# Optimization experiments

Hardware: AMD Instinct MI355X
Metric: run time of the kernel (lower is better)

The kernel has to match this reference:

```python
import jax, jax.numpy as jnp
import numpy as np

B, S, D = 4096, 200, 64
EPS = 1e-3  # keras BatchNormalization default epsilon

def setup_inputs() -> dict:
    key = jax.random.key(0)
    ks = jax.random.split(key, 8)
    return {
        "em": jax.random.normal(ks[0], (B, D), jnp.float32),
        "eu": jax.random.normal(ks[1], (B, D), jnp.float32),
        "Xu": jax.random.normal(ks[2], (B, S, D), jnp.float32),
        "W1": jax.random.normal(ks[3], (4 * D, 64), jnp.float32) * 0.05,
        "b1": jnp.zeros((64,), jnp.float32),
        "W2": jax.random.normal(ks[4], (64, 32), jnp.float32) * 0.1,
        "b2": jnp.zeros((32,), jnp.float32),
        "W3": jax.random.normal(ks[5], (32, 1), jnp.float32) * 0.1,
        "b3": jnp.zeros((1,), jnp.float32),
        "gamma": jnp.ones((2 * D,), jnp.float32),
        "beta": jnp.zeros((2 * D,), jnp.float32),
        "mov_mean": jnp.zeros((2 * D,), jnp.float32),
        "mov_var": jnp.ones((2 * D,), jnp.float32),
    }

def reference(em, eu, Xu, W1, b1, W2, b2, W3, b3, gamma, beta, mov_mean, mov_var):
    # DIN attention: query = em tiled over seq, key = value = Xu
    q = jnp.broadcast_to(em[:, None, :], Xu.shape)            # [B,S,D]
    info = jnp.concatenate([q, Xu, q - Xu, q * Xu], axis=-1)  # [B,S,4D]
    h = jax.nn.relu(info @ W1 + b1)                           # [B,S,64]
    h = jax.nn.relu(h @ W2 + b2)                              # [B,S,32]
    logits = (h @ W3 + b3)[..., 0]                            # [B,S]
    w = jax.nn.softmax(logits, axis=-1)                       # [B,S]
    pooled = jnp.einsum('bs,bsd->bd', w, Xu)                  # [B,D]
    info_all = jnp.concatenate([pooled, em], axis=-1)         # [B,2D]
    bn = (info_all - mov_mean) * jax.lax.rsqrt(mov_var + EPS) * gamma + beta
    return jnp.concatenate([bn, eu], axis=-1)                 # [B,2D+Du]
```

## Files before the change

### kernel.cpp

```cpp
#include <hip/hip_runtime.h>
#include <hip/hip_bf16.h>
#include <math.h>

typedef __bf16 bf16_t;
typedef bf16_t bf16x4 __attribute__((ext_vector_type(4)));
typedef bf16_t bf16x8 __attribute__((ext_vector_type(8)));
typedef float  f32x4  __attribute__((ext_vector_type(4)));

#define SEQ 200
#define SP  208
#define DD  64
#define RS  72

#define MFMA(a, b, c) __builtin_amdgcn_mfma_f32_16x16x32_bf16((a), (b), (c), 0, 0, 0)

__global__ __launch_bounds__(256) void prep_kernel(
    const float* __restrict__ em, const float* __restrict__ W1,
    const float* __restrict__ b1, const float* __restrict__ W2,
    bf16_t* __restrict__ Wbc, bf16_t* __restrict__ W1dt,
    bf16_t* __restrict__ W2t, float* __restrict__ Q)
{
  const int tid = threadIdx.x;
  if (blockIdx.x == 0) {
    for (int i = tid; i < 64 * 64; i += 256) {
      int n = i >> 6, k = i & 63;
      Wbc[i]  = (bf16_t)(W1[(64 + k) * 64 + n] - W1[(128 + k) * 64 + n]);
      W1dt[i] = (bf16_t)(W1[(192 + k) * 64 + n]);
    }
    for (int i = tid; i < 32 * 64; i += 256) {
      int n = i >> 6, k = i & 63;
      W2t[i] = (bf16_t)(W2[k * 32 + n]);
    }
  } else {
    int b = (blockIdx.x - 1) * 4 + (tid >> 6);
    int n = tid & 63;
    float acc = b1[n];
    for (int d = 0; d < 64; ++d)
      acc += em[(size_t)b * 64 + d] * (W1[d * 64 + n] + W1[(128 + d) * 64 + n]);
    Q[(size_t)b * 64 + n] = acc;
  }
}

__global__ __launch_bounds__(256, 4) void din_kernel(
    const float* __restrict__ em, const float* __restrict__ eu,
    const float* __restrict__ Xu, const float* __restrict__ b2,
    const float* __restrict__ W3, const float* __restrict__ b3,
    const float* __restrict__ gam, const float* __restrict__ bet,
    const float* __restrict__ mmean, const float* __restrict__ mvar,
    const bf16_t* __restrict__ Wbc, const bf16_t* __restrict__ W1dt,
    const bf16_t* __restrict__ W2t, const float* __restrict__ Q,
    float* __restrict__ out)
{
  __shared__ __align__(16) bf16_t A[SP * RS];
  __shared__ float logits[SP];
  __shared__ float red[8];
  float* part = (float*)A;

  const int tid  = threadIdx.x;
  const int b    = blockIdx.x;
  const int lane = tid & 63;
  const int wid  = tid >> 6;
  const int g    = lane >> 4;
  const int l16  = lane & 15;
  const int n1   = 16 * wid + l16;

  for (int i = tid; i < 8 * DD; i += 256) {
    int r = SEQ + (i >> 6), c = i & 63;
    A[r * RS + c] = (bf16_t)0.f;
  }

  const float4* Xr = (const float4*)(Xu + (size_t)b * SEQ * DD);
  float4 xg[13];
  #pragma unroll
  for (int k = 0; k < 12; ++k) xg[k] = Xr[tid + 256 * k];
  xg[12] = (tid < 128) ? Xr[tid + 3072] : make_float4(0.f, 0.f, 0.f, 0.f);

  const bf16x8* Wbc8  = (const bf16x8*)Wbc;
  const bf16x8* W1dt8 = (const bf16x8*)W1dt;
  const bf16x8* W2t8  = (const bf16x8*)W2t;
  bf16x8 bB[2];
  #pragma unroll
  for (int c = 0; c < 2; ++c) {
    bf16x8 wbc = Wbc8[n1 * 8 + 4 * c + g];
    bf16x8 w1d = W1dt8[n1 * 8 + 4 * c + g];
    float4 e0 = *(const float4*)&em[(size_t)b * DD + 32 * c + 8 * g];
    float4 e1 = *(const float4*)&em[(size_t)b * DD + 32 * c + 8 * g + 4];
    bB[c][0] = (bf16_t)((float)wbc[0] + e0.x * (float)w1d[0]);
    bB[c][1] = (bf16_t)((float)wbc[1] + e0.y * (float)w1d[1]);
    bB[c][2] = (bf16_t)((float)wbc[2] + e0.z * (float)w1d[2]);
    bB[c][3] = (bf16_t)((float)wbc[3] + e0.w * (float)w1d[3]);
    bB[c][4] = (bf16_t)((float)wbc[4] + e1.x * (float)w1d[4]);
    bB[c][5] = (bf16_t)((float)wbc[5] + e1.y * (float)w1d[5]);
    bB[c][6] = (bf16_t)((float)wbc[6] + e1.z * (float)w1d[6]);
    bB[c][7] = (bf16_t)((float)wbc[7] + e1.w * (float)w1d[7]);
  }
  const float qn   = Q[(size_t)b * DD + n1];
  const float b2v0 = b2[l16], b2v1 = b2[16 + l16];
  const float w3v0 = W3[l16], w3v1 = W3[16 + l16];
  const float b3s  = b3[0];

  bf16x4 xr[13];
  #pragma unroll
  for (int k = 0; k < 13; ++k) {
    bf16x4 xa;
    xa[0] = (bf16_t)xg[k].x; xa[1] = (bf16_t)xg[k].y;
    xa[2] = (bf16_t)xg[k].z; xa[3] = (bf16_t)xg[k].w;
    xr[k] = xa;
    int v = tid + 256 * k;
    if (v < SEQ * DD / 4)
      *(bf16x4*)&A[(v >> 4) * RS + (v & 15) * 4] = xa;
  }
  __syncthreads();

  f32x4 acc[13];
  #pragma unroll
  for (int t = 0; t < 13; ++t) {
    int rb = (16 * t + l16) * RS + 8 * g;
    bf16x8 a0 = *(const bf16x8*)&A[rb];
    bf16x8 a1 = *(const bf16x8*)&A[rb + 32];
    f32x4 a = {0.f, 0.f, 0.f, 0.f};
    a = MFMA(a0, bB[0], a);
    a = MFMA(a1, bB[1], a);
    acc[t] = a;
  }
  __syncthreads();

  #pragma unroll
  for (int t = 0; t < 13; ++t)
    #pragma unroll
    for (int r = 0; r < 4; ++r) {
      float v = acc[t][r] + qn;
      v = v > 0.f ? v : 0.f;
      A[(16 * t + 4 * g + r) * RS + n1] = (bf16_t)v;
    }
  __syncthreads();

  bf16x8 bW2f[2][2];
  #pragma unroll
  for (int c = 0; c < 2; ++c)
    #pragma unroll
    for (int u = 0; u < 2; ++u)
      bW2f[c][u] = W2t8[(16 * u + l16) * 8 + 4 * c + g];

  for (int t = wid; t < 13; t += 4) {
    int rb = (16 * t + l16) * RS + 8 * g;
    bf16x8 h0 = *(const bf16x8*)&A[rb];
    bf16x8 h1 = *(const bf16x8*)&A[rb + 32];
    f32x4 a0 = {0.f, 0.f, 0.f, 0.f}, a1 = {0.f, 0.f, 0.f, 0.f};
    a0 = MFMA(h0, bW2f[0][0], a0);
    a0 = MFMA(h1, bW2f[1][0], a0);
    a1 = MFMA(h0, bW2f[0][1], a1);
    a1 = MFMA(h1, bW2f[1][1], a1);
    #pragma unroll
    for (int r = 0; r < 4; ++r) {
      float p0 = fmaxf(a0[r] + b2v0, 0.f) * w3v0;
      float p1 = fmaxf(a1[r] + b2v1, 0.f) * w3v1;
      float pr = p0 + p1;
      pr += __shfl_xor(pr, 1);
      pr += __shfl_xor(pr, 2);
      pr += __shfl_xor(pr, 4);
      pr += __shfl_xor(pr, 8);
      if (l16 == 0) logits[16 * t + 4 * g + r] = pr + b3s;
    }
  }
  __syncthreads();

  float lv = (tid < SEQ) ? logits[tid] : -INFINITY;
  float mx = lv;
  #pragma unroll
  for (int o = 32; o > 0; o >>= 1) mx = fmaxf(mx, __shfl_xor(mx, o));
  if (lane == 0) red[wid] = mx;
  __syncthreads();
  mx = fmaxf(fmaxf(red[0], red[1]), fmaxf(red[2], red[3]));
  float e = (tid < SEQ) ? __expf(lv - mx) : 0.f;
  if (tid < SEQ) logits[tid] = e;
  float ssum = e;
  #pragma unroll
  for (int o = 32; o > 0; o >>= 1) ssum += __shfl_xor(ssum, o);
  if (lane == 0) red[4 + wid] = ssum;
  __syncthreads();
  const float inv = 1.f / (red[4] + red[5] + red[6] + red[7]);

  {
    float4 ps = {0.f, 0.f, 0.f, 0.f};
    #pragma unroll
    for (int k = 0; k < 13; ++k) {
      int v = tid + 256 * k;
      if (v < SEQ * DD / 4) {
        float w = logits[(tid >> 4) + 16 * k] * inv;
        ps.x += w * (float)xr[k][0];
        ps.y += w * (float)xr[k][1];
        ps.z += w * (float)xr[k][2];
        ps.w += w * (float)xr[k][3];
      }
    }
    *(float4*)&part[(tid >> 4) * 68 + (tid & 15) * 4] = ps;
  }
  __syncthreads();

  if (tid < 192) {
    float v;
    if (tid < 128) {
      float x;
      if (tid < 64) {
        x = 0.f;
        #pragma unroll
        for (int r = 0; r < 16; ++r) x += part[r * 68 + tid];
      } else {
        x = em[(size_t)b * DD + (tid - 64)];
      }
      v = (x - mmean[tid]) * rsqrtf(mvar[tid] + 1e-3f) * gam[tid] + bet[tid];
    } else {
      v = eu[(size_t)b * DD + (tid - 128)];
    }
    out[(size_t)b * 192 + tid] = v;
  }
}

extern "C" void kernel_launch(void* const* d_in, const int* in_sizes, int n_in,
                              void* d_out, int out_size, void* d_ws, size_t ws_size,
                              hipStream_t stream) {
  const float* em = (const float*)d_in[0];
  const float* eu = (const float*)d_in[1];
  const float* Xu = (const float*)d_in[2];
  const float* W1 = (const float*)d_in[3];
  const float* b1 = (const float*)d_in[4];
  const float* W2 = (const float*)d_in[5];
  const float* b2 = (const float*)d_in[6];
  const float* W3 = (const float*)d_in[7];
  const float* b3 = (const float*)d_in[8];
  const float* ga = (const float*)d_in[9];
  const float* be = (const float*)d_in[10];
  const float* mm = (const float*)d_in[11];
  const float* mv = (const float*)d_in[12];
  int B = in_sizes[0] / DD;

  float*  Q    = (float*)d_ws;
  bf16_t* Wbc  = (bf16_t*)((char*)d_ws + (size_t)B * 64 * 4);
  bf16_t* W1dt = Wbc  + 64 * 64;
  bf16_t* W2t  = W1dt + 64 * 64;

  prep_kernel<<<1 + B / 4, 256, 0, stream>>>(em, W1, b1, W2, Wbc, W1dt, W2t, Q);
  din_kernel<<<B, 256, 0, stream>>>(em, eu, Xu, b2, W3, b3, ga, be, mm, mv,
                                    Wbc, W1dt, W2t, Q, (float*)d_out);
}
```

Baseline: 326.5 us.

## Map one batch row per wavefront with streaming online softmax over sequence tiles

Each wavefront now processes a whole batch row, looping over 16-row sequence tiles. Every tile is loaded directly from global memory into MFMA fragments, and a running max/sum (flash-style online softmax) accumulates the pooled vector. This removes the block-wide __syncthreads barriers, the full-sequence LDS staging, and the separate softmax pass. b3 is dropped because a constant shift cancels in softmax. In exchange, each wave performs its tile loads serially with less latency hiding from intra-block overlap, uses more registers for the four N-tiles of B fragments, and pays extra exp/rescale work per tile.

```diff
diff --git a/kernel.cpp b/kernel.cpp
--- a/kernel.cpp
+++ b/kernel.cpp
@@ -8,9 +8,8 @@
 typedef float  f32x4  __attribute__((ext_vector_type(4)));
 
 #define SEQ 200
-#define SP  208
 #define DD  64
-#define RS  72
+#define NT  13
 
 #define MFMA(a, b, c) __builtin_amdgcn_mfma_f32_16x16x32_bf16((a), (b), (c), 0, 0, 0)
 
@@ -44,177 +43,180 @@
 __global__ __launch_bounds__(256, 4) void din_kernel(
     const float* __restrict__ em, const float* __restrict__ eu,
     const float* __restrict__ Xu, const float* __restrict__ b2,
-    const float* __restrict__ W3, const float* __restrict__ b3,
-    const float* __restrict__ gam, const float* __restrict__ bet,
-    const float* __restrict__ mmean, const float* __restrict__ mvar,
-    const bf16_t* __restrict__ Wbc, const bf16_t* __restrict__ W1dt,
-    const bf16_t* __restrict__ W2t, const float* __restrict__ Q,
-    float* __restrict__ out)
+    const float* __restrict__ W3, const float* __restrict__ gam,
+    const float* __restrict__ bet, const float* __restrict__ mmean,
+    const float* __restrict__ mvar, const bf16_t* __restrict__ Wbc,
+    const bf16_t* __restrict__ W1dt, const bf16_t* __restrict__ W2t,
+    const float* __restrict__ Q, float* __restrict__ out)
 {
-  __shared__ __align__(16) bf16_t A[SP * RS];
-  __shared__ float logits[SP];
-  __shared__ float red[8];
-  float* part = (float*)A;
+  __shared__ __align__(16) unsigned char lds[4 * 4416];
 
   const int tid  = threadIdx.x;
-  const int b    = blockIdx.x;
+  const int wid  = tid >> 6;
   const int lane = tid & 63;
-  const int wid  = tid >> 6;
   const int g    = lane >> 4;
   const int l16  = lane & 15;
-  const int n1   = 16 * wid + l16;
-
-  for (int i = tid; i < 8 * DD; i += 256) {
-    int r = SEQ + (i >> 6), c = i & 63;
-    A[r * RS + c] = (bf16_t)0.f;
-  }
-
-  const float4* Xr = (const float4*)(Xu + (size_t)b * SEQ * DD);
-  float4 xg[13];
-  #pragma unroll
-  for (int k = 0; k < 12; ++k) xg[k] = Xr[tid + 256 * k];
-  xg[12] = (tid < 128) ? Xr[tid + 3072] : make_float4(0.f, 0.f, 0.f, 0.f);
+  const int b    = blockIdx.x * 4 + wid;
+
+  bf16_t* h1   = (bf16_t*)(lds + wid * 4416);
+  float*  pool = (float*)(lds + wid * 4416);
+  float*  lam  = (float*)(lds + wid * 4416 + 4352);
 
   const bf16x8* Wbc8  = (const bf16x8*)Wbc;
   const bf16x8* W1dt8 = (const bf16x8*)W1dt;
   const bf16x8* W2t8  = (const bf16x8*)W2t;
-  bf16x8 bB[2];
+
+  float eml[2][8];
   #pragma unroll
   for (int c = 0; c < 2; ++c) {
-    bf16x8 wbc = Wbc8[n1 * 8 + 4 * c + g];
-    bf16x8 w1d = W1dt8[n1 * 8 + 4 * c + g];
     float4 e0 = *(const float4*)&em[(size_t)b * DD + 32 * c + 8 * g];
     float4 e1 = *(const float4*)&em[(size_t)b * DD + 32 * c + 8 * g + 4];
-    bB[c][0] = (bf16_t)((float)wbc[0] + e0.x * (float)w1d[0]);
-    bB[c][1] = (bf16_t)((float)wbc[1] + e0.y * (float)w1d[1]);
-    bB[c][2] = (bf16_t)((float)wbc[2] + e0.z * (float)w1d[2]);
-    bB[c][3] = (bf16_t)((float)wbc[3] + e0.w * (float)w1d[3]);
-    bB[c][4] = (bf16_t)((float)wbc[4] + e1.x * (float)w1d[4]);
-    bB[c][5] = (bf16_t)((float)wbc[5] + e1.y * (float)w1d[5]);
-    bB[c][6] = (bf16_t)((float)wbc[6] + e1.z * (float)w1d[6]);
-    bB[c][7] = (bf16_t)((float)wbc[7] + e1.w * (float)w1d[7]);
-  }
-  const float qn   = Q[(size_t)b * DD + n1];
+    eml[c][0] = e0.x; eml[c][1] = e0.y; eml[c][2] = e0.z; eml[c][3] = e0.w;
+    eml[c][4] = e1.x; eml[c][5] = e1.y; eml[c][6] = e1.z; eml[c][7] = e1.w;
+  }
+  bf16x8 bB[4][2];
+  #pragma unroll
+  for (int nt = 0; nt < 4; ++nt) {
+    int n = nt * 16 + l16;
+    #pragma unroll
+    for (int c = 0; c < 2; ++c) {
+      bf16x8 wbc = Wbc8[n * 8 + 4 * c + g];
+      bf16x8 w1d = W1dt8[n * 8 + 4 * c + g];
+      #pragma unroll
+      for (int j = 0; j < 8; ++j)
+        bB[nt][c][j] = (bf16_t)((float)wbc[j] + eml[c][j] * (float)w1d[j]);
+    }
+  }
+  bf16x8 bW2[2][2];
+  #pragma unroll
+  for (int c = 0; c < 2; ++c)
+    #pragma unroll
+    for (int u = 0; u < 2; ++u)
+      bW2[c][u] = W2t8[(16 * u + l16) * 8 + 4 * c + g];
+
+  float qv[4];
+  #pragma unroll
+  for (int nt = 0; nt < 4; ++nt) qv[nt] = Q[(size_t)b * DD + nt * 16 + l16];
   const float b2v0 = b2[l16], b2v1 = b2[16 + l16];
   const float w3v0 = W3[l16], w3v1 = W3[16 + l16];
-  const float b3s  = b3[0];
-
-  bf16x4 xr[13];
-  #pragma unroll
-  for (int k = 0; k < 13; ++k) {
-    bf16x4 xa;
-    xa[0] = (bf16_t)xg[k].x; xa[1] = (bf16_t)xg[k].y;
-    xa[2] = (bf16_t)xg[k].z; xa[3] = (bf16_t)xg[k].w;
-    xr[k] = xa;
-    int v = tid + 256 * k;
-    if (v < SEQ * DD / 4)
-      *(bf16x4*)&A[(v >> 4) * RS + (v & 15) * 4] = xa;
-  }
-  __syncthreads();
-
-  f32x4 acc[13];
-  #pragma unroll
-  for (int t = 0; t < 13; ++t) {
-    int rb = (16 * t + l16) * RS + 8 * g;
-    bf16x8 a0 = *(const bf16x8*)&A[rb];
-    bf16x8 a1 = *(const bf16x8*)&A[rb + 32];
-    f32x4 a = {0.f, 0.f, 0.f, 0.f};
-    a = MFMA(a0, bB[0], a);
-    a = MFMA(a1, bB[1], a);
-    acc[t] = a;
-  }
-  __syncthreads();
-
-  #pragma unroll
-  for (int t = 0; t < 13; ++t)
+
+  float m = -INFINITY, l = 0.f;
+  float pacc[2][8];
+  #pragma unroll
+  for (int c = 0; c < 2; ++c)
+    #pragma unroll
+    for (int j = 0; j < 8; ++j) pacc[c][j] = 0.f;
+
+  const float* Xbase = Xu + (size_t)b * SEQ * DD;
+
+  for (int t = 0; t < NT; ++t) {
+    const int s = 16 * t + l16;
+    bf16x8 xf[2];
+    if (s < SEQ) {
+      const float* Xr = Xbase + (size_t)s * DD;
+      #pragma unroll
+      for (int c = 0; c < 2; ++c) {
+        float4 x0 = *(const float4*)&Xr[32 * c + 8 * g];
+        float4 x1 = *(const float4*)&Xr[32 * c + 8 * g + 4];
+        xf[c][0] = (bf16_t)x0.x; xf[c][1] = (bf16_t)x0.y;
+        xf[c][2] = (bf16_t)x0.z; xf[c][3] = (bf16_t)x0.w;
+        xf[c][4] = (bf16_t)x1.x; xf[c][5] = (bf16_t)x1.y;
+        xf[c][6] = (bf16_t)x1.z; xf[c][7] = (bf16_t)x1.w;
+      }
+    } else {
+      #pragma unroll
+      for (int c = 0; c < 2; ++c)
+        #pragma unroll
+        for (int j = 0; j < 8; ++j) xf[c][j] = (bf16_t)0.f;
+    }
+
+    f32x4 a1[4];
+    #pragma unroll
+    for (int nt = 0; nt < 4; ++nt) {
+      f32x4 a = {0.f, 0.f, 0.f, 0.f};
+      a = MFMA(xf[0], bB[nt][0], a);
+      a = MFMA(xf[1], bB[nt][1], a);
+      a1[nt] = a;
+    }
+    #pragma unroll
+    for (int nt = 0; nt < 4; ++nt)
+      #pragma unroll
+      for (int r = 0; r < 4; ++r) {
+        float v = a1[nt][r] + qv[nt];
+        v = v > 0.f ? v : 0.f;
+        h1[(4 * g + r) * 72 + nt * 16 + l16] = (bf16_t)v;
+      }
+
+    bf16x8 h0 = *(const bf16x8*)&h1[l16 * 72 + 8 * g];
+    bf16x8 h1f = *(const bf16x8*)&h1[l16 * 72 + 32 + 8 * g];
+    f32x4 a20 = {0.f, 0.f, 0.f, 0.f}, a21 = {0.f, 0.f, 0.f, 0.f};
+    a20 = MFMA(h0, bW2[0][0], a20);
+    a20 = MFMA(h1f, bW2[1][0], a20);
+    a21 = MFMA(h0, bW2[0][1], a21);
+    a21 = MFMA(h1f, bW2[1][1], a21);
+
     #pragma unroll
     for (int r = 0; r < 4; ++r) {
-      float v = acc[t][r] + qn;
-      v = v > 0.f ? v : 0.f;
-      A[(16 * t + 4 * g + r) * RS + n1] = (bf16_t)v;
-    }
-  __syncthreads();
-
-  bf16x8 bW2f[2][2];
-  #pragma unroll
-  for (int c = 0; c < 2; ++c)
-    #pragma unroll
-    for (int u = 0; u < 2; ++u)
-      bW2f[c][u] = W2t8[(16 * u + l16) * 8 + 4 * c + g];
-
-  for (int t = wid; t < 13; t += 4) {
-    int rb = (16 * t + l16) * RS + 8 * g;
-    bf16x8 h0 = *(const bf16x8*)&A[rb];
-    bf16x8 h1 = *(const bf16x8*)&A[rb + 32];
-    f32x4 a0 = {0.f, 0.f, 0.f, 0.f}, a1 = {0.f, 0.f, 0.f, 0.f};
-    a0 = MFMA(h0, bW2f[0][0], a0);
-    a0 = MFMA(h1, bW2f[1][0], a0);
-    a1 = MFMA(h0, bW2f[0][1], a1);
-    a1 = MFMA(h1, bW2f[1][1], a1);
-    #pragma unroll
-    for (int r = 0; r < 4; ++r) {
-      float p0 = fmaxf(a0[r] + b2v0, 0.f) * w3v0;
-      float p1 = fmaxf(a1[r] + b2v1, 0.f) * w3v1;
+      float p0 = fmaxf(a20[r] + b2v0, 0.f) * w3v0;
+      float p1 = fmaxf(a21[r] + b2v1, 0.f) * w3v1;
       float pr = p0 + p1;
       pr += __shfl_xor(pr, 1);
       pr += __shfl_xor(pr, 2);
       pr += __shfl_xor(pr, 4);
       pr += __shfl_xor(pr, 8);
-      if (l16 == 0) logits[16 * t + 4 * g + r] = pr + b3s;
-    }
-  }
-  __syncthreads();
-
-  float lv = (tid < SEQ) ? logits[tid] : -INFINITY;
-  float mx = lv;
-  #pragma unroll
-  for (int o = 32; o > 0; o >>= 1) mx = fmaxf(mx, __shfl_xor(mx, o));
-  if (lane == 0) red[wid] = mx;
-  __syncthreads();
-  mx = fmaxf(fmaxf(red[0], red[1]), fmaxf(red[2], red[3]));
-  float e = (tid < SEQ) ? __expf(lv - mx) : 0.f;
-  if (tid < SEQ) logits[tid] = e;
-  float ssum = e;
-  #pragma unroll
-  for (int o = 32; o > 0; o >>= 1) ssum += __shfl_xor(ssum, o);
-  if (lane == 0) red[4 + wid] = ssum;
-  __syncthreads();
-  const float inv = 1.f / (red[4] + red[5] + red[6] + red[7]);
+      if (l16 == 0) {
+        int row = 4 * g + r;
+        lam[row] = (16 * t + row < SEQ) ? pr : -INFINITY;
+      }
+    }
+    float lv = lam[l16];
+    float mt = lv;
+    mt = fmaxf(mt, __shfl_xor(mt, 1));
+    mt = fmaxf(mt, __shfl_xor(mt, 2));
+    mt = fmaxf(mt, __shfl_xor(mt, 4));
+    mt = fmaxf(mt, __shfl_xor(mt, 8));
+
+    float mn = fmaxf(m, mt);
+    float alpha = __expf(m - mn);
+    float e = __expf(lv - mn);
+    float es = e;
+    es += __shfl_xor(es, 1);
+    es += __shfl_xor(es, 2);
+    es += __shfl_xor(es, 4);
+    es += __shfl_xor(es, 8);
+    l = l * alpha + es;
+    #pragma unroll
+    for (int c = 0; c < 2; ++c)
+      #pragma unroll
+      for (int j = 0; j < 8; ++j)
+        pacc[c][j] = pacc[c][j] * alpha + e * (float)xf[c][j];
+    m = mn;
+  }
 
   {
-    float4 ps = {0.f, 0.f, 0.f, 0.f};
-    #pragma unroll
-    for (int k = 0; k < 13; ++k) {
-      int v = tid + 256 * k;
-      if (v < SEQ * DD / 4) {
-        float w = logits[(tid >> 4) + 16 * k] * inv;
-        ps.x += w * (float)xr[k][0];
-        ps.y += w * (float)xr[k][1];
-        ps.z += w * (float)xr[k][2];
-        ps.w += w * (float)xr[k][3];
-      }
-    }
-    *(float4*)&part[(tid >> 4) * 68 + (tid & 15) * 4] = ps;
-  }
-  __syncthreads();
-
-  if (tid < 192) {
-    float v;
-    if (tid < 128) {
-      float x;
-      if (tid < 64) {
-        x = 0.f;
-        #pragma unroll
-        for (int r = 0; r < 16; ++r) x += part[r * 68 + tid];
-      } else {
-        x = em[(size_t)b * DD + (tid - 64)];
-      }
-      v = (x - mmean[tid]) * rsqrtf(mvar[tid] + 1e-3f) * gam[tid] + bet[tid];
-    } else {
-      v = eu[(size_t)b * DD + (tid - 128)];
-    }
-    out[(size_t)b * 192 + tid] = v;
-  }
+    f32x4 p;
+    p[0] = pacc[0][0]; p[1] = pacc[0][1]; p[2] = pacc[0][2]; p[3] = pacc[0][3];
+    *(f32x4*)&pool[l16 * 68 + 8 * g] = p;
+    p[0] = pacc[0][4]; p[1] = pacc[0][5]; p[2] = pacc[0][6]; p[3] = pacc[0][7];
+    *(f32x4*)&pool[l16 * 68 + 8 * g + 4] = p;
+    p[0] = pacc[1][0]; p[1] = pacc[1][1]; p[2] = pacc[1][2]; p[3] = pacc[1][3];
+    *(f32x4*)&pool[l16 * 68 + 32 + 8 * g] = p;
+    p[0] = pacc[1][4]; p[1] = pacc[1][5]; p[2] = pacc[1][6]; p[3] = pacc[1][7];
+    *(f32x4*)&pool[l16 * 68 + 32 + 8 * g + 4] = p;
+  }
+  float ps = 0.f;
+  #pragma unroll
+  for (int r = 0; r < 16; ++r) ps += pool[r * 68 + lane];
+  const float pooled = ps * (1.f / l);
+
+  const size_t ob = (size_t)b * 192;
+  out[ob + lane] =
+      (pooled - mmean[lane]) * rsqrtf(mvar[lane] + 1e-3f) * gam[lane] + bet[lane];
+  float emv = em[(size_t)b * DD + lane];
+  out[ob + 64 + lane] =
+      (emv - mmean[64 + lane]) * rsqrtf(mvar[64 + lane] + 1e-3f) * gam[64 + lane] +
+      bet[64 + lane];
+  out[ob + 128 + lane] = eu[(size_t)b * DD + lane];
 }
 
 extern "C" void kernel_launch(void* const* d_in, const int* in_sizes, int n_in,
@@ -228,7 +230,6 @@
   const float* W2 = (const float*)d_in[5];
   const float* b2 = (const float*)d_in[6];
   const float* W3 = (const float*)d_in[7];
-  const float* b3 = (const float*)d_in[8];
   const float* ga = (const float*)d_in[9];
   const float* be = (const float*)d_in[10];
   const float* mm = (const float*)d_in[11];
@@ -241,6 +242,6 @@
   bf16_t* W2t  = W1dt + 64 * 64;
 
   prep_kernel<<<1 + B / 4, 256, 0, stream>>>(em, W1, b1, W2, Wbc, W1dt, W2t, Q);
-  din_kernel<<<B, 256, 0, stream>>>(em, eu, Xu, b2, W3, b3, ga, be, mm, mv,
-                                    Wbc, W1dt, W2t, Q, (float*)d_out);
+  din_kernel<<<B / 4, 256, 0, stream>>>(em, eu, Xu, b2, W3, ga, be, mm, mv,
+                                        Wbc, W1dt, W2t, Q, (float*)d_out);
 }
```

Result: slower. 339.3 us (+3.9%).
